# Kernel tuning notes

Hardware: AMD Instinct MI355X
Metric: run time of the kernel (lower is better)

## Reference

```python
import jax, jax.numpy as jnp
import numpy as np

H = 512
B = 64
S = 2048
NUM_LAYERS = 1


def setup_inputs() -> dict:
    key = jax.random.key(0)
    ks = jax.random.split(key, 8)
    scale = 1.0 / np.sqrt(H)
    return {
        "hidden": jax.random.normal(ks[0], (NUM_LAYERS, B, H), dtype=jnp.float32),
        "encoder_outputs": jax.random.normal(ks[1], (B, S, H), dtype=jnp.float32),
        "U_w": jax.random.uniform(ks[2], (H, H), jnp.float32, -scale, scale),
        "U_b": jax.random.uniform(ks[3], (H,), jnp.float32, -scale, scale),
        "W_w": jax.random.uniform(ks[4], (H, H), jnp.float32, -scale, scale),
        "W_b": jax.random.uniform(ks[5], (H,), jnp.float32, -scale, scale),
        "V_w": jax.random.uniform(ks[6], (1, H), jnp.float32, -scale, scale),
        "V_b": jax.random.uniform(ks[7], (1,), jnp.float32, -scale, scale),
    }


def reference(hidden, encoder_outputs, U_w, U_b, W_w, W_b, V_w, V_b):
    # hidden: [L, B, H] -> take last layer, like hidden[-1]
    h = hidden[-1]  # [B, H]
    # Uatt(h): [B, H] -> broadcast over src_len
    u = h @ U_w.T + U_b            # [B, H]
    w = jnp.einsum('bsh,kh->bsk', encoder_outputs, W_w) + W_b  # [B, S, H]
    combined = jnp.tanh(u[:, None, :] + w)                     # [B, S, H]
    energy = jnp.einsum('bsh,h->bs', combined, V_w[0]) + V_b[0]  # [B, S]
    attn = jax.nn.softmax(energy, axis=1)                       # [B, S]
    context = jnp.einsum('bs,bsh->bh', attn, encoder_outputs)   # [B, H]
    return (context, attn)
```

## Files before the change

### kernel.cpp

```cpp
#include <hip/hip_runtime.h>
#include <hip/hip_bf16.h>

#define H 512
#define B 64
#define S 2048

#define BM 128
#define BN 128
#define BK 32

typedef __bf16 bf16x8 __attribute__((ext_vector_type(8)));
typedef float f32x4 __attribute__((ext_vector_type(4)));

__device__ __forceinline__ unsigned cvt2(float x, float y) {
    union { __hip_bfloat162 h; unsigned u; } cv;
    cv.h = __float22bfloat162_rn(make_float2(x, y));
    return cv.u;
}

__device__ __forceinline__ float fast_tanh(float x) {
    float e = __expf(2.0f * x);
    float r = __builtin_amdgcn_rcpf(e + 1.0f);
    return 1.0f - 2.0f * r;
}

__global__ void u_kernel(const float* __restrict__ hid, const float* __restrict__ Uw,
                         const float* __restrict__ Ub, const float* __restrict__ Wb,
                         float* __restrict__ u) {
    __shared__ float sh[H];
    int b = blockIdx.x;
    int t = threadIdx.x;
    sh[t] = hid[b * H + t];
    __syncthreads();
    const float4* row = (const float4*)(Uw + (size_t)t * H);
    float acc = 0.f;
    #pragma unroll 4
    for (int i = 0; i < H / 4; ++i) {
        float4 w4 = row[i];
        acc += w4.x * sh[4 * i] + w4.y * sh[4 * i + 1] + w4.z * sh[4 * i + 2] + w4.w * sh[4 * i + 3];
    }
    u[b * H + t] = acc + Ub[t] + Wb[t];
}

__global__ __launch_bounds__(256) void energy_kernel(
        const float* __restrict__ enc, const float* __restrict__ Ww,
        const float* __restrict__ Vw, const float* __restrict__ u,
        float* __restrict__ energy) {
    const int kt = blockIdx.x;
    const int st = blockIdx.y;
    const int b  = blockIdx.z;
    const int k0 = kt * BN;
    const int s0 = st * BM;
    const int tid  = threadIdx.x;
    const int wave = tid >> 6;
    const int lane = tid & 63;
    const int wr = wave >> 1, wc = wave & 1;
    const int quad = lane >> 4, c = lane & 15;

    __shared__ unsigned short As[BM][BK];
    __shared__ unsigned short Bs[BN][BK];
    __shared__ float uS[BN], vS[BN];

    if (tid < BN) { uS[tid] = u[b * H + k0 + tid]; vS[tid] = Vw[k0 + tid]; }

    f32x4 acc[4][4] = {};

    const float* Abase = enc + ((size_t)(b * S + s0)) * H;
    const float* Bbase = Ww + (size_t)k0 * H;

    for (int kk = 0; kk < H / BK; ++kk) {
        const int h0 = kk * BK;
        __syncthreads();
        #pragma unroll
        for (int i = 0; i < 4; ++i) {
            int f   = tid + i * 256;
            int row = f >> 3;
            int c4  = (f & 7) * 4;
            float4 a4 = *(const float4*)(Abase + (size_t)row * H + h0 + c4);
            float4 b4 = *(const float4*)(Bbase + (size_t)row * H + h0 + c4);
            uint2 ap, bp;
            ap.x = cvt2(a4.x, a4.y); ap.y = cvt2(a4.z, a4.w);
            bp.x = cvt2(b4.x, b4.y); bp.y = cvt2(b4.z, b4.w);
            *(uint2*)&As[row][c4] = ap;
            *(uint2*)&Bs[row][c4] = bp;
        }
        __syncthreads();
        bf16x8 af[4], bfr[4];
        #pragma unroll
        for (int i = 0; i < 4; ++i) af[i]  = *(const bf16x8*)&As[wr * 64 + i * 16 + c][quad * 8];
        #pragma unroll
        for (int j = 0; j < 4; ++j) bfr[j] = *(const bf16x8*)&Bs[wc * 64 + j * 16 + c][quad * 8];
        #pragma unroll
        for (int i = 0; i < 4; ++i)
            #pragma unroll
            for (int j = 0; j < 4; ++j)
                acc[i][j] = __builtin_amdgcn_mfma_f32_16x16x32_bf16(af[i], bfr[j], acc[i][j], 0, 0, 0);
    }

    float* erow = energy + b * S + s0;
    #pragma unroll
    for (int i = 0; i < 4; ++i) {
        #pragma unroll
        for (int r = 0; r < 4; ++r) {
            float esum = 0.f;
            #pragma unroll
            for (int j = 0; j < 4; ++j) {
                int col = wc * 64 + j * 16 + c;
                esum += vS[col] * fast_tanh(uS[col] + acc[i][j][r]);
            }
            esum += __shfl_xor(esum, 1, 64);
            esum += __shfl_xor(esum, 2, 64);
            esum += __shfl_xor(esum, 4, 64);
            esum += __shfl_xor(esum, 8, 64);
            if (c == 0) atomicAdd(&erow[wr * 64 + i * 16 + quad * 4 + r], esum);
        }
    }
}

__global__ void softmax_kernel(const float* __restrict__ energy, float* __restrict__ attn) {
    int b = blockIdx.x;
    int t = threadIdx.x;
    const float* e = energy + b * S;
    float v[8];
    float m = -1e30f;
    #pragma unroll
    for (int i = 0; i < 8; ++i) { v[i] = e[t + i * 256]; m = fmaxf(m, v[i]); }
    #pragma unroll
    for (int off = 1; off < 64; off <<= 1) m = fmaxf(m, __shfl_xor(m, off, 64));
    __shared__ float redm[4], reds[4];
    if ((t & 63) == 0) redm[t >> 6] = m;
    __syncthreads();
    m = fmaxf(fmaxf(redm[0], redm[1]), fmaxf(redm[2], redm[3]));
    float s = 0.f;
    #pragma unroll
    for (int i = 0; i < 8; ++i) { v[i] = __expf(v[i] - m); s += v[i]; }
    #pragma unroll
    for (int off = 1; off < 64; off <<= 1) s += __shfl_xor(s, off, 64);
    if ((t & 63) == 0) reds[t >> 6] = s;
    __syncthreads();
    float inv = 1.0f / (reds[0] + reds[1] + reds[2] + reds[3]);
    #pragma unroll
    for (int i = 0; i < 8; ++i) attn[b * S + t + i * 256] = v[i] * inv;
}

#define CCHUNK 256
__global__ void context_kernel(const float* __restrict__ enc, const float* __restrict__ attn,
                               float* __restrict__ ctx) {
    int b  = blockIdx.x >> 3;
    int ch = blockIdx.x & 7;
    int t  = threadIdx.x;
    __shared__ float aS[CCHUNK];
    aS[t] = attn[b * S + ch * CCHUNK + t];
    __syncthreads();
    const float* ebase = enc + ((size_t)(b * S + ch * CCHUNK)) * H + t;
    float c0 = 0.f, c1 = 0.f;
    #pragma unroll 4
    for (int s = 0; s < CCHUNK; ++s) {
        float a = aS[s];
        c0 += a * ebase[(size_t)s * H];
        c1 += a * ebase[(size_t)s * H + 256];
    }
    atomicAdd(&ctx[b * H + t], c0);
    atomicAdd(&ctx[b * H + t + 256], c1);
}

extern "C" void kernel_launch(void* const* d_in, const int* in_sizes, int n_in,
                              void* d_out, int out_size, void* d_ws, size_t ws_size,
                              hipStream_t stream) {
    (void)in_sizes; (void)n_in; (void)out_size; (void)ws_size;
    const float* hid = (const float*)d_in[0];
    const float* enc = (const float*)d_in[1];
    const float* Uw  = (const float*)d_in[2];
    const float* Ub  = (const float*)d_in[3];
    const float* Ww  = (const float*)d_in[4];
    const float* Wb  = (const float*)d_in[5];
    const float* Vw  = (const float*)d_in[6];

    float* out_ctx  = (float*)d_out;
    float* out_attn = out_ctx + B * H;
    float* energy   = (float*)d_ws;
    float* u        = energy + B * S;

    hipMemsetAsync(d_out, 0, (size_t)B * H * sizeof(float), stream);
    hipMemsetAsync(energy, 0, (size_t)B * S * sizeof(float), stream);

    u_kernel<<<B, H, 0, stream>>>(hid, Uw, Ub, Wb, u);
    energy_kernel<<<dim3(4, 16, B), 256, 0, stream>>>(enc, Ww, Vw, u, energy);
    softmax_kernel<<<B, 256, 0, stream>>>(energy, out_attn);
    context_kernel<<<B * 8, 256, 0, stream>>>(enc, out_attn, out_ctx);
}
```

Baseline: 560.8 us.

## Loop energy kernel over all hidden tiles, prefetch loads, warp-reduce u kernel

```diff
diff --git a/kernel.cpp b/kernel.cpp
--- a/kernel.cpp
+++ b/kernel.cpp
@@ -24,32 +24,30 @@
     return 1.0f - 2.0f * r;
 }
 
-__global__ void u_kernel(const float* __restrict__ hid, const float* __restrict__ Uw,
-                         const float* __restrict__ Ub, const float* __restrict__ Wb,
-                         float* __restrict__ u) {
-    __shared__ float sh[H];
-    int b = blockIdx.x;
-    int t = threadIdx.x;
-    sh[t] = hid[b * H + t];
-    __syncthreads();
-    const float4* row = (const float4*)(Uw + (size_t)t * H);
-    float acc = 0.f;
-    #pragma unroll 4
-    for (int i = 0; i < H / 4; ++i) {
-        float4 w4 = row[i];
-        acc += w4.x * sh[4 * i] + w4.y * sh[4 * i + 1] + w4.z * sh[4 * i + 2] + w4.w * sh[4 * i + 3];
-    }
-    u[b * H + t] = acc + Ub[t] + Wb[t];
+__global__ __launch_bounds__(256) void u_kernel(
+        const float* __restrict__ hid, const float* __restrict__ Uw,
+        const float* __restrict__ Ub, const float* __restrict__ Wb,
+        float* __restrict__ u) {
+    const int b = blockIdx.y;
+    const int k = blockIdx.x * 4 + (threadIdx.x >> 6);
+    const int lane = threadIdx.x & 63;
+    const float4* wrow = (const float4*)(Uw + (size_t)k * H);
+    const float4* hrow = (const float4*)(hid + (size_t)b * H);
+    float4 w0 = wrow[lane * 2], w1 = wrow[lane * 2 + 1];
+    float4 h0 = hrow[lane * 2], h1 = hrow[lane * 2 + 1];
+    float acc = w0.x * h0.x + w0.y * h0.y + w0.z * h0.z + w0.w * h0.w
+              + w1.x * h1.x + w1.y * h1.y + w1.z * h1.z + w1.w * h1.w;
+    #pragma unroll
+    for (int off = 1; off < 64; off <<= 1) acc += __shfl_xor(acc, off, 64);
+    if (lane == 0) u[b * H + k] = acc + Ub[k] + Wb[k];
 }
 
 __global__ __launch_bounds__(256) void energy_kernel(
         const float* __restrict__ enc, const float* __restrict__ Ww,
         const float* __restrict__ Vw, const float* __restrict__ u,
         float* __restrict__ energy) {
-    const int kt = blockIdx.x;
-    const int st = blockIdx.y;
-    const int b  = blockIdx.z;
-    const int k0 = kt * BN;
+    const int st = blockIdx.x;
+    const int b  = blockIdx.y;
     const int s0 = st * BM;
     const int tid  = threadIdx.x;
     const int wave = tid >> 6;
@@ -59,61 +57,103 @@
 
     __shared__ unsigned short As[BM][BK];
     __shared__ unsigned short Bs[BN][BK];
-    __shared__ float uS[BN], vS[BN];
-
-    if (tid < BN) { uS[tid] = u[b * H + k0 + tid]; vS[tid] = Vw[k0 + tid]; }
-
-    f32x4 acc[4][4] = {};
-
-    const float* Abase = enc + ((size_t)(b * S + s0)) * H;
-    const float* Bbase = Ww + (size_t)k0 * H;
-
-    for (int kk = 0; kk < H / BK; ++kk) {
-        const int h0 = kk * BK;
-        __syncthreads();
+    __shared__ float uS[H], vS[H];
+    __shared__ float red[BM];
+
+    #pragma unroll
+    for (int i = tid; i < H; i += 256) { uS[i] = u[b * H + i]; vS[i] = Vw[i]; }
+
+    const int srow = tid >> 3;
+    const int sc4  = (tid & 7) * 4;
+    const float* pA = enc + ((size_t)(b * S + s0) + srow) * H + sc4;
+
+    float esum[4][4] = {};
+
+    for (int kt = 0; kt < 4; ++kt) {
+        const float* pB = Ww + ((size_t)(kt * BN) + srow) * H + sc4;
+        f32x4 acc[4][4] = {};
+
+        float4 pa[4], pb[4];
         #pragma unroll
         for (int i = 0; i < 4; ++i) {
-            int f   = tid + i * 256;
-            int row = f >> 3;
-            int c4  = (f & 7) * 4;
-            float4 a4 = *(const float4*)(Abase + (size_t)row * H + h0 + c4);
-            float4 b4 = *(const float4*)(Bbase + (size_t)row * H + h0 + c4);
-            uint2 ap, bp;
-            ap.x = cvt2(a4.x, a4.y); ap.y = cvt2(a4.z, a4.w);
-            bp.x = cvt2(b4.x, b4.y); bp.y = cvt2(b4.z, b4.w);
-            *(uint2*)&As[row][c4] = ap;
-            *(uint2*)&Bs[row][c4] = bp;
+            pa[i] = *(const float4*)(pA + (size_t)i * 32 * H);
+            pb[i] = *(const float4*)(pB + (size_t)i * 32 * H);
         }
-        __syncthreads();
-        bf16x8 af[4], bfr[4];
-        #pragma unroll
-        for (int i = 0; i < 4; ++i) af[i]  = *(const bf16x8*)&As[wr * 64 + i * 16 + c][quad * 8];
-        #pragma unroll
-        for (int j = 0; j < 4; ++j) bfr[j] = *(const bf16x8*)&Bs[wc * 64 + j * 16 + c][quad * 8];
+
+        for (int kk = 0; kk < H / BK; ++kk) {
+            uint2 ap[4], bp[4];
+            #pragma unroll
+            for (int i = 0; i < 4; ++i) {
+                ap[i].x = cvt2(pa[i].x, pa[i].y); ap[i].y = cvt2(pa[i].z, pa[i].w);
+                bp[i].x = cvt2(pb[i].x, pb[i].y); bp[i].y = cvt2(pb[i].z, pb[i].w);
+            }
+            __syncthreads();
+            #pragma unroll
+            for (int i = 0; i < 4; ++i) {
+                *(uint2*)&As[srow + i * 32][sc4] = ap[i];
+                *(uint2*)&Bs[srow + i * 32][sc4] = bp[i];
+            }
+            __syncthreads();
+            if (kk < H / BK - 1) {
+                const int h0 = (kk + 1) * BK;
+                #pragma unroll
+                for (int i = 0; i < 4; ++i) {
+                    pa[i] = *(const float4*)(pA + (size_t)i * 32 * H + h0);
+                    pb[i] = *(const float4*)(pB + (size_t)i * 32 * H + h0);
+                }
+            }
+            bf16x8 af[4], bfr[4];
+            #pragma unroll
+            for (int i = 0; i < 4; ++i) af[i]  = *(const bf16x8*)&As[wr * 64 + i * 16 + c][quad * 8];
+            #pragma unroll
+            for (int j = 0; j < 4; ++j) bfr[j] = *(const bf16x8*)&Bs[wc * 64 + j * 16 + c][quad * 8];
+            #pragma unroll
+            for (int i = 0; i < 4; ++i)
+                #pragma unroll
+                for (int j = 0; j < 4; ++j)
+                    acc[i][j] = __builtin_amdgcn_mfma_f32_16x16x32_bf16(af[i], bfr[j], acc[i][j], 0, 0, 0);
+        }
+
         #pragma unroll
         for (int i = 0; i < 4; ++i)
             #pragma unroll
-            for (int j = 0; j < 4; ++j)
-                acc[i][j] = __builtin_amdgcn_mfma_f32_16x16x32_bf16(af[i], bfr[j], acc[i][j], 0, 0, 0);
-    }
-
-    float* erow = energy + b * S + s0;
-    #pragma unroll
-    for (int i = 0; i < 4; ++i) {
+            for (int j = 0; j < 4; ++j) {
+                const int col = kt * BN + wc * 64 + j * 16 + c;
+                const float v = vS[col], uu = uS[col];
+                #pragma unroll
+                for (int r = 0; r < 4; ++r)
+                    esum[i][r] += v * fast_tanh(uu + acc[i][j][r]);
+            }
+    }
+
+    #pragma unroll
+    for (int i = 0; i < 4; ++i)
         #pragma unroll
         for (int r = 0; r < 4; ++r) {
-            float esum = 0.f;
-            #pragma unroll
-            for (int j = 0; j < 4; ++j) {
-                int col = wc * 64 + j * 16 + c;
-                esum += vS[col] * fast_tanh(uS[col] + acc[i][j][r]);
-            }
-            esum += __shfl_xor(esum, 1, 64);
-            esum += __shfl_xor(esum, 2, 64);
-            esum += __shfl_xor(esum, 4, 64);
-            esum += __shfl_xor(esum, 8, 64);
-            if (c == 0) atomicAdd(&erow[wr * 64 + i * 16 + quad * 4 + r], esum);
+            float e = esum[i][r];
+            e += __shfl_xor(e, 1, 64);
+            e += __shfl_xor(e, 2, 64);
+            e += __shfl_xor(e, 4, 64);
+            e += __shfl_xor(e, 8, 64);
+            esum[i][r] = e;
         }
+    __syncthreads();
+    if (wc == 0 && c == 0) {
+        #pragma unroll
+        for (int i = 0; i < 4; ++i)
+            #pragma unroll
+            for (int r = 0; r < 4; ++r)
+                red[wr * 64 + i * 16 + quad * 4 + r] = esum[i][r];
+    }
+    __syncthreads();
+    if (wc == 1 && c == 0) {
+        #pragma unroll
+        for (int i = 0; i < 4; ++i)
+            #pragma unroll
+            for (int r = 0; r < 4; ++r) {
+                const int row = wr * 64 + i * 16 + quad * 4 + r;
+                energy[b * S + s0 + row] = red[row] + esum[i][r];
+            }
     }
 }
 
@@ -143,18 +183,19 @@
     for (int i = 0; i < 8; ++i) attn[b * S + t + i * 256] = v[i] * inv;
 }
 
-#define CCHUNK 256
-__global__ void context_kernel(const float* __restrict__ enc, const float* __restrict__ attn,
-                               float* __restrict__ ctx) {
-    int b  = blockIdx.x >> 3;
-    int ch = blockIdx.x & 7;
+#define CCHUNK 128
+__global__ __launch_bounds__(256) void context_kernel(
+        const float* __restrict__ enc, const float* __restrict__ attn,
+        float* __restrict__ ctx) {
+    int b  = blockIdx.x >> 4;
+    int ch = blockIdx.x & 15;
     int t  = threadIdx.x;
     __shared__ float aS[CCHUNK];
-    aS[t] = attn[b * S + ch * CCHUNK + t];
+    if (t < CCHUNK) aS[t] = attn[b * S + ch * CCHUNK + t];
     __syncthreads();
     const float* ebase = enc + ((size_t)(b * S + ch * CCHUNK)) * H + t;
     float c0 = 0.f, c1 = 0.f;
-    #pragma unroll 4
+    #pragma unroll 8
     for (int s = 0; s < CCHUNK; ++s) {
         float a = aS[s];
         c0 += a * ebase[(size_t)s * H];
@@ -182,10 +223,9 @@
     float* u        = energy + B * S;
 
     hipMemsetAsync(d_out, 0, (size_t)B * H * sizeof(float), stream);
-    hipMemsetAsync(energy, 0, (size_t)B * S * sizeof(float), stream);
-
-    u_kernel<<<B, H, 0, stream>>>(hid, Uw, Ub, Wb, u);
-    energy_kernel<<<dim3(4, 16, B), 256, 0, stream>>>(enc, Ww, Vw, u, energy);
+
+    u_kernel<<<dim3(H / 4, B), 256, 0, stream>>>(hid, Uw, Ub, Wb, u);
+    energy_kernel<<<dim3(S / BM, B), 256, 0, stream>>>(enc, Ww, Vw, u, energy);
     softmax_kernel<<<B, 256, 0, stream>>>(energy, out_attn);
-    context_kernel<<<B * 8, 256, 0, stream>>>(enc, out_attn, out_ctx);
-}
+    context_kernel<<<B * (S / CCHUNK), 256, 0, stream>>>(enc, out_attn, out_ctx);
+}
```

New measurement: 549.5 us. 2.0% less time.
